# Kernel optimization log

Hardware: AMD Instinct MI355X
Metric: run time of the kernel (lower is better)

## Reference

```python
import jax, jax.numpy as jnp
import numpy as np

# Module config (init_kwargs)
CIN, COUT, KH, KW = 256, 256, 3, 3
STRIDE, PADDING = 1, 1
T = 64                 # psum chunk size along the reduction (K) axis
NBITS = 8              # saturating accumulator bits (signed)
QMAX = (1 << (NBITS - 1)) - 1   # 127
QMIN = QMAX - (1 << NBITS) + 1  # -128


def setup_inputs() -> dict:
    key = jax.random.key(0)
    k1, k2 = jax.random.split(key)
    x = jax.random.normal(k1, (8, CIN, 56, 56), dtype=jnp.float32)
    # nn.Parameter(torch.rand((N,1)) * 0.001)
    weights = jax.random.uniform(k2, (CIN * COUT * KH * KW, 1), dtype=jnp.float32) * 0.001
    return {"x": x, "weights": weights}


def reference(x, weights):
    B, _, H, W = x.shape
    OH = (H - KH + 2 * PADDING) // STRIDE + 1
    OW = (W - KW + 2 * PADDING) // STRIDE + 1

    w = weights.reshape(COUT, CIN, KH, KW)
    # per-output-channel scaling factor, detached
    scale = jax.lax.stop_gradient(jnp.mean(jnp.abs(w), axis=(1, 2, 3), keepdims=True))
    # binarize with STE: sign(w).detach() - clamp(w).detach() + clamp(w)
    wc = jnp.clip(w, -1.0, 1.0)
    wb = jax.lax.stop_gradient(jnp.sign(w) - wc) + wc

    # unfold (im2col); channel varies slowest -> matches torch.nn.functional.unfold
    patches = jax.lax.conv_general_dilated_patches(
        x, (KH, KW), (STRIDE, STRIDE), [(PADDING, PADDING), (PADDING, PADDING)]
    )  # [B, CIN*KH*KW, OH*OW... (spatial)]
    K = CIN * KH * KW
    L = OH * OW
    A = patches.reshape(B, K, L).transpose(0, 2, 1)  # [B, L, K]
    X = wb.reshape(COUT, K).T                        # [K, COUT]

    pad = (-K) % T
    if pad:
        A = jnp.pad(A, ((0, 0), (0, 0), (0, pad)))
        X = jnp.pad(X, ((0, pad), (0, 0)))
    nT = (K + pad) // T

    A4 = A.reshape(B, L, nT, T)        # chunked reduction axis
    X3 = X.reshape(nT, T, COUT)
    # per-chunk partial sums (satmm_cuda.forward_psum)
    psum = jnp.einsum('blnt,ntc->nblc', A4, X3)  # [nT, B, L, COUT]

    # saturating sequential accumulation: reduce(lambda a,b: clip(a+b, QMIN, QMAX))
    def step(carry, p):
        return jnp.clip(carry + p, QMIN, QMAX), None
    y_flat, _ = jax.lax.scan(step, psum[0], psum[1:])  # [B, L, COUT]

    y = y_flat.transpose(0, 2, 1).reshape(B, COUT, OH, OW)
    y = y * scale.reshape(1, -1, 1, 1)
    # psum returned in the original [B, L, COUT, nT] layout
    return y, psum.transpose(1, 2, 3, 0)
```

## Files before the change

### kernel.cpp

```cpp
#include <hip/hip_runtime.h>
#include <hip/hip_bf16.h>

#define CIN 256
#define COUT 256
#define HW 56
#define BATCH 8
#define L_SPATIAL 3136
#define K_TOTAL 2304
#define NT 36
#define NH 18
#define ROWF (COUT * NT)
#define KSTRIDE 2312
#define ATILE_BYTES (16 * KSTRIDE * 2)
#define LDS_BYTES ATILE_BYTES
#define MT_TOTAL 1568
#define TILES_PER_IMG 196
#define QMAXF 127.0f
#define QMINF -128.0f

typedef short bf16x8 __attribute__((ext_vector_type(8)));
typedef float f32x4 __attribute__((ext_vector_type(4)));

__device__ __forceinline__ void nt_store4(float* p, f32x4 v) {
  __builtin_nontemporal_store(v, reinterpret_cast<f32x4*>(p));
}

__global__ __launch_bounds__(256) void prep_kernel(
    const float* __restrict__ w, unsigned short* __restrict__ bsign,
    float* __restrict__ scale) {
  const int c = blockIdx.x;
  const int t = threadIdx.x;
  const float* row = w + (size_t)c * K_TOTAL;
  unsigned short* out = bsign + (size_t)c * K_TOTAL;
  float acc = 0.0f;
#pragma unroll
  for (int j = 0; j < 9; ++j) {
    const int k = t + 256 * j;
    const float v = row[k];
    acc += __builtin_fabsf(v);
    out[k] = (v > 0.0f) ? (unsigned short)0x3F80
           : ((v < 0.0f) ? (unsigned short)0xBF80 : (unsigned short)0);
  }
#pragma unroll
  for (int o = 32; o > 0; o >>= 1) acc += __shfl_down(acc, o, 64);
  __shared__ float red[4];
  if ((t & 63) == 0) red[t >> 6] = acc;
  __syncthreads();
  if (t == 0) scale[c] = (red[0] + red[1] + red[2] + red[3]) * (1.0f / 2304.0f);
}

template <int H>
__device__ __forceinline__ void compute_half(
    const unsigned short* __restrict__ aptr,
    const unsigned short* __restrict__ bptr,
    f32x4* __restrict__ ps, f32x4& sacc) {
  const f32x4 zero = {0.0f, 0.0f, 0.0f, 0.0f};
  bf16x8 b0 = *reinterpret_cast<const bf16x8*>(bptr);
  bf16x8 b1 = *reinterpret_cast<const bf16x8*>(bptr + 32);
#pragma unroll
  for (int n = 0; n < NT; ++n) {
    bf16x8 nb0, nb1;
    if (n + 1 < NT) {
      nb0 = *reinterpret_cast<const bf16x8*>(bptr + (n + 1) * 64);
      nb1 = *reinterpret_cast<const bf16x8*>(bptr + (n + 1) * 64 + 32);
    }
    bf16x8 a0 = *reinterpret_cast<const bf16x8*>(aptr + n * 64);
    bf16x8 a1 = *reinterpret_cast<const bf16x8*>(aptr + n * 64 + 32);
    f32x4 acc = __builtin_amdgcn_mfma_f32_16x16x32_bf16(a0, b0, zero, 0, 0, 0);
    acc = __builtin_amdgcn_mfma_f32_16x16x32_bf16(a1, b1, acc, 0, 0, 0);
    if (n >= H * NH && n < (H + 1) * NH) ps[n - H * NH] = acc;
    if (n == 0) {
      sacc = acc;
    } else {
#pragma unroll
      for (int e = 0; e < 4; ++e)
        sacc[e] = __builtin_amdgcn_fmed3f(sacc[e] + acc[e], QMINF, QMAXF);
    }
    b0 = nb0;
    b1 = nb1;
  }
}

__global__ __launch_bounds__(512, 4) void satconv_kernel(
    const float* __restrict__ x, const unsigned short* __restrict__ bsign,
    const float* __restrict__ scale, float* __restrict__ y_out,
    float* __restrict__ psum_out) {
  extern __shared__ char smem[];
  unsigned short* Atile = (unsigned short*)smem;
  float* stage = (float*)smem;

  const int tid = threadIdx.x;
  const int bid = blockIdx.x;
  const int mt = bid % MT_TOTAL;
  const int cb = bid / MT_TOTAL;
  const int m_tile = (mt & 7) * TILES_PER_IMG + (mt >> 3);
  const int m0 = m_tile << 4;

  {
    const int ml = tid & 15;
    const int grp = tid >> 4;
    const int m = m0 + ml;
    const int b = m / L_SPATIAL;
    const int l = m - b * L_SPATIAL;
    const int oh = l / HW;
    const int ow = l - oh * HW;
    const float* xb = x + (size_t)b * (CIN * L_SPATIAL);
    unsigned short* arow = Atile + ml * KSTRIDE;
    for (int r = grp; r < 768; r += 32) {
      const int ci = r / 3;
      const int kh = r - ci * 3;
      const int h = oh + kh - 1;
      const bool hv = ((unsigned)h < (unsigned)HW);
      const float* xr = xb + (ci * HW + h) * HW;
      const int kb = ci * 9 + kh * 3;
#pragma unroll
      for (int kw = 0; kw < 3; ++kw) {
        const int wv = ow + kw - 1;
        float v = 0.0f;
        if (hv && ((unsigned)wv < (unsigned)HW)) v = xr[wv];
        __hip_bfloat16 bv = __float2bfloat16(v);
        arow[kb + kw] = *reinterpret_cast<unsigned short*>(&bv);
      }
    }
  }

  const int lane = tid & 63;
  const int wave = tid >> 6;
  const int cl = lane & 15;
  const int q = lane >> 4;
  const int cs = wave >> 1;
  const int h = wave & 1;
  const int c = (cb << 6) + (cs << 4) + cl;

  const float sc = scale[c];

  __syncthreads();

  const unsigned short* aptr = Atile + cl * KSTRIDE + q * 8;
  const unsigned short* bptr = bsign + (size_t)c * K_TOTAL + q * 8;
  const int b_img = m0 / L_SPATIAL;
  const int l0 = m0 - b_img * L_SPATIAL;

  f32x4 ps[NH];
  f32x4 sacc;
  if (h == 0) compute_half<0>(aptr, bptr, ps, sacc);
  else        compute_half<1>(aptr, bptr, ps, sacc);

  if (h == 0) {
    f32x4 yv;
#pragma unroll
    for (int e = 0; e < 4; ++e) yv[e] = sacc[e] * sc;
    nt_store4(y_out + ((size_t)b_img * COUT + c) * L_SPATIAL + l0 + (q << 2), yv);
  }

  __syncthreads();

#pragma unroll
  for (int r = 0; r < 2; ++r) {
    if ((cs >> 1) == r) {
      float* reg = stage + (cs & 1) * 9216;
      const int coldw = cl * 36 + h * NH;
#pragma unroll
      for (int j = 0; j < NH; ++j) {
#pragma unroll
        for (int e = 0; e < 4; ++e)
          reg[((q << 2) + e) * 576 + coldw + j] = ps[j][e];
      }
    }
    __syncthreads();
    {
      const int CS = wave >> 2;
      const int mrow0 = (wave & 3) << 2;
      const int cs_g = (r << 1) + CS;
      const float* lds_f = stage + wave * 2304;
      float* gbase = psum_out + (size_t)(m0 + mrow0) * ROWF
                   + ((cb << 6) + (cs_g << 4)) * 36;
#pragma unroll
      for (int i = 0; i < 9; ++i) {
        const int xx = i * 256 + (lane << 2);
        const int ml = xx / 576;
        const int roff = xx - ml * 576;
        f32x4 v = *reinterpret_cast<const f32x4*>(lds_f + xx);
        nt_store4(gbase + (size_t)ml * ROWF + roff, v);
      }
    }
    __syncthreads();
  }
}

extern "C" void kernel_launch(void* const* d_in, const int* in_sizes, int n_in,
                              void* d_out, int out_size, void* d_ws, size_t ws_size,
                              hipStream_t stream) {
  const float* x = (const float*)d_in[0];
  const float* w = (const float*)d_in[1];
  float* y = (float*)d_out;
  float* psum = y + (size_t)BATCH * COUT * L_SPATIAL;
  unsigned short* bsign = (unsigned short*)d_ws;
  float* scale = (float*)((char*)d_ws + (size_t)COUT * K_TOTAL * 2);

  prep_kernel<<<COUT, 256, 0, stream>>>(w, bsign, scale);

  hipFuncSetAttribute(reinterpret_cast<const void*>(satconv_kernel),
                      hipFuncAttributeMaxDynamicSharedMemorySize, LDS_BYTES);
  satconv_kernel<<<MT_TOTAL * 4, 512, LDS_BYTES, stream>>>(
      x, bsign, scale, y, psum);
}
```

Baseline: 1.430 ms.

## Cover all output channels per M-tile block and split K chunks across wave pairs

Each block now handles all 256 output channels for one 16-row M tile, using 1024 threads and looping over two channel halves. Previously each M tile's im2col A tile was rebuilt in four separate blocks; now it is built once per tile, which removes that repeated gather and conversion. Within a wave pair, each wave computes only its own 18 of the 36 K chunks instead of both computing all 36. The saturating accumulation is carried between the two waves through a small LDS buffer. The psum staging moves to a separate LDS region with vectorized writes and precomputed global offsets. This raises LDS use to about 152KB per block and adds more barriers, which likely allows only one block per CU.

```diff
diff --git a/kernel.cpp b/kernel.cpp
--- a/kernel.cpp
+++ b/kernel.cpp
@@ -12,7 +12,9 @@
 #define ROWF (COUT * NT)
 #define KSTRIDE 2312
 #define ATILE_BYTES (16 * KSTRIDE * 2)
-#define LDS_BYTES ATILE_BYTES
+#define STAGE_OFF ATILE_BYTES
+#define CARRY_OFF (ATILE_BYTES + 73728)
+#define LDS_BYTES (CARRY_OFF + 8192)
 #define MT_TOTAL 1568
 #define TILES_PER_IMG 196
 #define QMAXF 127.0f
@@ -20,6 +22,7 @@
 
 typedef short bf16x8 __attribute__((ext_vector_type(8)));
 typedef float f32x4 __attribute__((ext_vector_type(4)));
+typedef float f32x2 __attribute__((ext_vector_type(2)));
 
 __device__ __forceinline__ void nt_store4(float* p, f32x4 v) {
   __builtin_nontemporal_store(v, reinterpret_cast<f32x4*>(p));
@@ -50,50 +53,53 @@
 }
 
 template <int H>
-__device__ __forceinline__ void compute_half(
+__device__ __forceinline__ void compute18(
     const unsigned short* __restrict__ aptr,
     const unsigned short* __restrict__ bptr,
     f32x4* __restrict__ ps, f32x4& sacc) {
   const f32x4 zero = {0.0f, 0.0f, 0.0f, 0.0f};
-  bf16x8 b0 = *reinterpret_cast<const bf16x8*>(bptr);
-  bf16x8 b1 = *reinterpret_cast<const bf16x8*>(bptr + 32);
-#pragma unroll
-  for (int n = 0; n < NT; ++n) {
+  const unsigned short* ap = aptr + H * NH * 64;
+  const unsigned short* bp = bptr + H * NH * 64;
+  bf16x8 b0 = *reinterpret_cast<const bf16x8*>(bp);
+  bf16x8 b1 = *reinterpret_cast<const bf16x8*>(bp + 32);
+#pragma unroll
+  for (int j = 0; j < NH; ++j) {
     bf16x8 nb0, nb1;
-    if (n + 1 < NT) {
-      nb0 = *reinterpret_cast<const bf16x8*>(bptr + (n + 1) * 64);
-      nb1 = *reinterpret_cast<const bf16x8*>(bptr + (n + 1) * 64 + 32);
-    }
-    bf16x8 a0 = *reinterpret_cast<const bf16x8*>(aptr + n * 64);
-    bf16x8 a1 = *reinterpret_cast<const bf16x8*>(aptr + n * 64 + 32);
+    if (j + 1 < NH) {
+      nb0 = *reinterpret_cast<const bf16x8*>(bp + (j + 1) * 64);
+      nb1 = *reinterpret_cast<const bf16x8*>(bp + (j + 1) * 64 + 32);
+    }
+    bf16x8 a0 = *reinterpret_cast<const bf16x8*>(ap + j * 64);
+    bf16x8 a1 = *reinterpret_cast<const bf16x8*>(ap + j * 64 + 32);
     f32x4 acc = __builtin_amdgcn_mfma_f32_16x16x32_bf16(a0, b0, zero, 0, 0, 0);
     acc = __builtin_amdgcn_mfma_f32_16x16x32_bf16(a1, b1, acc, 0, 0, 0);
-    if (n >= H * NH && n < (H + 1) * NH) ps[n - H * NH] = acc;
-    if (n == 0) {
-      sacc = acc;
-    } else {
-#pragma unroll
-      for (int e = 0; e < 4; ++e)
-        sacc[e] = __builtin_amdgcn_fmed3f(sacc[e] + acc[e], QMINF, QMAXF);
+    ps[j] = acc;
+    if (H == 0) {
+      if (j == 0) {
+        sacc = acc;
+      } else {
+#pragma unroll
+        for (int e = 0; e < 4; ++e)
+          sacc[e] = __builtin_amdgcn_fmed3f(sacc[e] + acc[e], QMINF, QMAXF);
+      }
     }
     b0 = nb0;
     b1 = nb1;
   }
 }
 
-__global__ __launch_bounds__(512, 4) void satconv_kernel(
+__global__ __launch_bounds__(1024, 4) void satconv_kernel(
     const float* __restrict__ x, const unsigned short* __restrict__ bsign,
     const float* __restrict__ scale, float* __restrict__ y_out,
     float* __restrict__ psum_out) {
   extern __shared__ char smem[];
   unsigned short* Atile = (unsigned short*)smem;
-  float* stage = (float*)smem;
+  float* stage = (float*)(smem + STAGE_OFF);
+  float* carryb = (float*)(smem + CARRY_OFF);
 
   const int tid = threadIdx.x;
   const int bid = blockIdx.x;
-  const int mt = bid % MT_TOTAL;
-  const int cb = bid / MT_TOTAL;
-  const int m_tile = (mt & 7) * TILES_PER_IMG + (mt >> 3);
+  const int m_tile = (bid & 7) * TILES_PER_IMG + (bid >> 3);
   const int m0 = m_tile << 4;
 
   {
@@ -106,12 +112,12 @@
     const int ow = l - oh * HW;
     const float* xb = x + (size_t)b * (CIN * L_SPATIAL);
     unsigned short* arow = Atile + ml * KSTRIDE;
-    for (int r = grp; r < 768; r += 32) {
+    for (int r = grp; r < 768; r += 64) {
       const int ci = r / 3;
       const int kh = r - ci * 3;
-      const int h = oh + kh - 1;
-      const bool hv = ((unsigned)h < (unsigned)HW);
-      const float* xr = xb + (ci * HW + h) * HW;
+      const int hh = oh + kh - 1;
+      const bool hv = ((unsigned)hh < (unsigned)HW);
+      const float* xr = xb + (ci * HW + hh) * HW;
       const int kb = ci * 9 + kh * 3;
 #pragma unroll
       for (int kw = 0; kw < 3; ++kw) {
@@ -130,61 +136,97 @@
   const int q = lane >> 4;
   const int cs = wave >> 1;
   const int h = wave & 1;
-  const int c = (cb << 6) + (cs << 4) + cl;
-
-  const float sc = scale[c];
+
+  const float sc_s0 = scale[cs * 16 + cl];
+  const float sc_s1 = scale[128 + cs * 16 + cl];
+
+  int base_it[9];
+  {
+#pragma unroll
+    for (int it = 0; it < 9; ++it) {
+      const int f = it * 256 + lane * 4;
+      const int qq = f / 576;
+      const int rem = f - qq * 576;
+      const int ci = rem / 36;
+      const int n0 = rem - ci * 36;
+      base_it[it] = ((m0 + (qq << 2)) * COUT + ci) * NT + n0;
+    }
+  }
 
   __syncthreads();
 
   const unsigned short* aptr = Atile + cl * KSTRIDE + q * 8;
-  const unsigned short* bptr = bsign + (size_t)c * K_TOTAL + q * 8;
   const int b_img = m0 / L_SPATIAL;
   const int l0 = m0 - b_img * L_SPATIAL;
-
-  f32x4 ps[NH];
-  f32x4 sacc;
-  if (h == 0) compute_half<0>(aptr, bptr, ps, sacc);
-  else        compute_half<1>(aptr, bptr, ps, sacc);
-
-  if (h == 0) {
-    f32x4 yv;
-#pragma unroll
-    for (int e = 0; e < 4; ++e) yv[e] = sacc[e] * sc;
-    nt_store4(y_out + ((size_t)b_img * COUT + c) * L_SPATIAL + l0 + (q << 2), yv);
-  }
-
-  __syncthreads();
-
-#pragma unroll
-  for (int r = 0; r < 2; ++r) {
-    if ((cs >> 1) == r) {
-      float* reg = stage + (cs & 1) * 9216;
-      const int coldw = cl * 36 + h * NH;
+  float* reg = stage + cs * 2304;
+
+  for (int s = 0; s < 2; ++s) {
+    const int csub0 = (s << 7) + (cs << 4);
+    const int c = csub0 + cl;
+    const unsigned short* bptr = bsign + (size_t)c * K_TOTAL + q * 8;
+
+    f32x4 ps[NH];
+    f32x4 sacc = {0.0f, 0.0f, 0.0f, 0.0f};
+    if (h == 0) compute18<0>(aptr, bptr, ps, sacc);
+    else        compute18<1>(aptr, bptr, ps, sacc);
+
+    if (h == 0)
+      *reinterpret_cast<f32x4*>(carryb + cs * 256 + lane * 4) = sacc;
+    __syncthreads();
+    if (h == 1) {
+      f32x4 cin = *reinterpret_cast<const f32x4*>(carryb + cs * 256 + lane * 4);
 #pragma unroll
       for (int j = 0; j < NH; ++j) {
 #pragma unroll
         for (int e = 0; e < 4; ++e)
-          reg[((q << 2) + e) * 576 + coldw + j] = ps[j][e];
-      }
-    }
-    __syncthreads();
-    {
-      const int CS = wave >> 2;
-      const int mrow0 = (wave & 3) << 2;
-      const int cs_g = (r << 1) + CS;
-      const float* lds_f = stage + wave * 2304;
-      float* gbase = psum_out + (size_t)(m0 + mrow0) * ROWF
-                   + ((cb << 6) + (cs_g << 4)) * 36;
-#pragma unroll
-      for (int i = 0; i < 9; ++i) {
-        const int xx = i * 256 + (lane << 2);
-        const int ml = xx / 576;
-        const int roff = xx - ml * 576;
-        f32x4 v = *reinterpret_cast<const f32x4*>(lds_f + xx);
-        nt_store4(gbase + (size_t)ml * ROWF + roff, v);
-      }
-    }
-    __syncthreads();
+          cin[e] = __builtin_amdgcn_fmed3f(cin[e] + ps[j][e], QMINF, QMAXF);
+      }
+      const float sc = (s == 0) ? sc_s0 : sc_s1;
+      f32x4 yv;
+#pragma unroll
+      for (int e = 0; e < 4; ++e) yv[e] = cin[e] * sc;
+      nt_store4(y_out + ((size_t)b_img * COUT + c) * L_SPATIAL + l0 + (q << 2), yv);
+    }
+
+    const int soff = csub0 * NT;
+#pragma unroll
+    for (int rg = 0; rg < 4; ++rg) {
+      {
+        float* wr = reg + q * 576 + cl * 36 + h * NH;
+        if (h == 0) {
+          f32x4 v;
+#pragma unroll
+          for (int g = 0; g < 4; ++g) {
+            v[0] = ps[4 * g + 0][rg]; v[1] = ps[4 * g + 1][rg];
+            v[2] = ps[4 * g + 2][rg]; v[3] = ps[4 * g + 3][rg];
+            *reinterpret_cast<f32x4*>(wr + 4 * g) = v;
+          }
+          f32x2 t = {ps[16][rg], ps[17][rg]};
+          *reinterpret_cast<f32x2*>(wr + 16) = t;
+        } else {
+          f32x2 t = {ps[0][rg], ps[1][rg]};
+          *reinterpret_cast<f32x2*>(wr) = t;
+          f32x4 v;
+#pragma unroll
+          for (int g = 0; g < 4; ++g) {
+            v[0] = ps[4 * g + 2][rg]; v[1] = ps[4 * g + 3][rg];
+            v[2] = ps[4 * g + 4][rg]; v[3] = ps[4 * g + 5][rg];
+            *reinterpret_cast<f32x4*>(wr + 2 + 4 * g) = v;
+          }
+        }
+      }
+      __syncthreads();
+      {
+        const int rgoff = rg * ROWF + soff;
+        const int it0 = (h == 0) ? 0 : 5;
+        const int it1 = (h == 0) ? 5 : 9;
+        for (int it = it0; it < it1; ++it) {
+          f32x4 v = *reinterpret_cast<const f32x4*>(reg + it * 256 + lane * 4);
+          nt_store4(psum_out + (size_t)(base_it[it] + rgoff), v);
+        }
+      }
+      __syncthreads();
+    }
   }
 }
 
@@ -202,6 +244,6 @@
 
   hipFuncSetAttribute(reinterpret_cast<const void*>(satconv_kernel),
                       hipFuncAttributeMaxDynamicSharedMemorySize, LDS_BYTES);
-  satconv_kernel<<<MT_TOTAL * 4, 512, LDS_BYTES, stream>>>(
+  satconv_kernel<<<MT_TOTAL, 1024, LDS_BYTES, stream>>>(
       x, bsign, scale, y, psum);
 }
```

Measured after the change: 1.196 ms. 1.2x faster.
